# Performance work log

Measured on AMD Instinct MI355X. Metric: run time of the kernel, lower is better.

## Reference

```python
import jax, jax.numpy as jnp
import numpy as np

DECAY = 0.99
EPS = 1e-5
NUM_EMBEDDINGS = 8192


def setup_inputs() -> dict:
    key = jax.random.key(0)
    k1, k2 = jax.random.split(key)
    N, D, K = 65536, 64, NUM_EMBEDDINGS
    x = jax.random.normal(k1, (N, D), dtype=jnp.float32)
    vq_embedding = jax.random.uniform(k2, (K, D), dtype=jnp.float32)
    vq_cluster_size = jnp.ones((K,), dtype=jnp.float32)
    return {"x": x, "vq_embedding": vq_embedding, "vq_cluster_size": vq_cluster_size}


def reference(x, vq_embedding, vq_cluster_size):
    N, D = x.shape
    K = vq_embedding.shape[0]

    # BatchNorm1d(affine=False), training mode: normalize with batch stats (biased var)
    mean = jnp.mean(x, axis=0)                      # [D]
    var = jnp.var(x, axis=0)                        # biased, [D]
    xn = (x - mean) / jnp.sqrt(var + EPS)           # [N, D]

    # pairwise squared distances [N, K]
    distances = (jnp.sum(xn * xn, axis=1, keepdims=True)
                 + jnp.sum(vq_embedding * vq_embedding, axis=1)
                 - 2.0 * (xn @ vq_embedding.T))
    idx = jnp.argmin(distances, axis=1)             # [N]

    # one-hot scatter expressed as segment sums
    dw = jax.ops.segment_sum(xn, idx, num_segments=K)                      # [K, D]
    counts = jax.ops.segment_sum(jnp.ones((N,), x.dtype), idx, num_segments=K)  # [K]

    # EMA codebook update
    new_emb = vq_cluster_size[:, None] * vq_embedding * DECAY + (1.0 - DECAY) * dw
    new_size = vq_cluster_size * DECAY + (1.0 - DECAY) * counts
    new_emb = new_emb / new_size[:, None]

    # BN running stats with momentum=None (cumulative avg, first batch):
    # running_mean = batch mean, running_var = unbiased batch var
    unbiased_var = var * (N / (N - 1))
    running_std = jnp.sqrt(unbiased_var + EPS)
    vq_embedding_output = new_emb * running_std[None, :] + mean[None, :]

    return vq_embedding_output, new_emb, new_size
```

## Files before the change

### kernel.cpp

```cpp
#include <hip/hip_runtime.h>

#define NROWS 65536
#define DIM 64
#define KCODES 8192
#define DECAYF 0.99f
#define EPSV 1e-5f
#define KD (KCODES * DIM)
#define KSPLIT 4
#define KC (KCODES / KSPLIT)
#define ROUNDS (KC / 128)

typedef _Float16 half8 __attribute__((ext_vector_type(8)));
typedef float f32x16 __attribute__((ext_vector_type(16)));

#define WS_STATS  0
#define WS_NHCK   256
#define WS_EBUF   8448
#define WS_PSUM   270592
#define WS_PSQ    286976
#define WS_PACKED 303360
#define WS_DW     368896
#define WS_COUNTS 893184
#define ZERO_F4   149504

__global__ __launch_bounds__(256) void k_prep_stats(
    const float* __restrict__ emb, const float* __restrict__ x,
    half8* __restrict__ ebuf, float* __restrict__ nhck,
    float* __restrict__ psum, float* __restrict__ psq,
    float4* __restrict__ zbase)
{
    const int tid = blockIdx.x * 256 + threadIdx.x;

    #pragma unroll
    for (int i = 0; i < 3; ++i) {
        int z = tid + i * 65536;
        if (z < ZERO_F4) zbase[z] = float4{0.f, 0.f, 0.f, 0.f};
    }

    {
        const int code = tid >> 3, sub = tid & 7;
        const int c = sub >> 1, h = sub & 1;
        const float* e = emb + (size_t)code * DIM + c * 16 + h * 8;
        float4 a = *(const float4*)e;
        float4 b = *(const float4*)(e + 4);
        float f[8] = {a.x, a.y, a.z, a.w, b.x, b.y, b.z, b.w};
        half8 hh;
        float ssq = 0.f;
        #pragma unroll
        for (int i = 0; i < 8; ++i) {
            hh[i] = (_Float16)(f[i] - 0.5f);
            ssq += f[i] * f[i];
        }
        #pragma unroll
        for (int o = 1; o < 8; o <<= 1) ssq += __shfl_xor(ssq, o, 64);
        if (sub == 0) nhck[code] = 10.6875f - 0.5f * ssq;
        const int R = code >> 7, t = (code >> 5) & 3, col = code & 31;
        ebuf[(size_t)R * 1024 + t * 256 + c * 64 + h * 32 + col] = hh;
    }

    {
        const int wave = threadIdx.x >> 6;
        const int col  = threadIdx.x & 63;
        const int base = blockIdx.x * 256;
        float s = 0.f, q = 0.f;
        #pragma unroll 4
        for (int i = 0; i < 64; ++i) {
            int r = base + i * 4 + wave;
            float v = x[(size_t)r * DIM + col];
            s += v;
            q += v * v;
        }
        __shared__ float ls[4][64];
        __shared__ float lq[4][64];
        ls[wave][col] = s;
        lq[wave][col] = q;
        __syncthreads();
        if (threadIdx.x < 64) {
            psum[blockIdx.x * 64 + col] = ls[0][col] + ls[1][col] + ls[2][col] + ls[3][col];
            psq[blockIdx.x * 64 + col]  = lq[0][col] + lq[1][col] + lq[2][col] + lq[3][col];
        }
    }
}

__global__ __launch_bounds__(256) void k_colstats_final(
    const float* __restrict__ psum, const float* __restrict__ psq,
    float* __restrict__ stats)
{
    const int col = threadIdx.x & 63, part = threadIdx.x >> 6;
    float s = 0.f, q = 0.f;
    for (int i = part * 64; i < part * 64 + 64; ++i) {
        s += psum[i * 64 + col];
        q += psq[i * 64 + col];
    }
    __shared__ float ls[4][64];
    __shared__ float lq[4][64];
    ls[part][col] = s;
    lq[part][col] = q;
    __syncthreads();
    if (threadIdx.x < 64) {
        s = ls[0][col] + ls[1][col] + ls[2][col] + ls[3][col];
        q = lq[0][col] + lq[1][col] + lq[2][col] + lq[3][col];
        const float n = (float)NROWS;
        float mean = s / n;
        float var = q / n - mean * mean;
        if (var < 0.f) var = 0.f;
        stats[col]       = mean;
        stats[64 + col]  = 1.0f / sqrtf(var + EPSV);
        stats[128 + col] = sqrtf(var * (n / (n - 1.0f)) + EPSV);
    }
}

__device__ __forceinline__ void gload16(const void* g, void* l)
{
    __builtin_amdgcn_global_load_lds(
        (const __attribute__((address_space(1))) void*)g,
        (__attribute__((address_space(3))) void*)l, 16, 0, 0);
}

__device__ __forceinline__ void build_afrag(const float* __restrict__ xr,
                                            const float* __restrict__ stats,
                                            int h, half8* a)
{
    #pragma unroll
    for (int c = 0; c < 4; ++c) {
        const int d = c * 16 + h * 8;
        float4 v0 = *(const float4*)(xr + d);
        float4 v1 = *(const float4*)(xr + d + 4);
        float4 m0 = *(const float4*)(stats + d);
        float4 m1 = *(const float4*)(stats + d + 4);
        float4 s0 = *(const float4*)(stats + 64 + d);
        float4 s1 = *(const float4*)(stats + 64 + d + 4);
        a[c][0] = (_Float16)((v0.x - m0.x) * s0.x);
        a[c][1] = (_Float16)((v0.y - m0.y) * s0.y);
        a[c][2] = (_Float16)((v0.z - m0.z) * s0.z);
        a[c][3] = (_Float16)((v0.w - m0.w) * s0.w);
        a[c][4] = (_Float16)((v1.x - m1.x) * s1.x);
        a[c][5] = (_Float16)((v1.y - m1.y) * s1.y);
        a[c][6] = (_Float16)((v1.z - m1.z) * s1.z);
        a[c][7] = (_Float16)((v1.w - m1.w) * s1.w);
    }
}

__global__ __launch_bounds__(256) void k_argmin32(
    const float* __restrict__ x, const half8* __restrict__ ebuf,
    const float* __restrict__ nhckg, const float* __restrict__ stats,
    unsigned* __restrict__ packed)
{
    __shared__ half8 smem[2048];

    const int lane = threadIdx.x & 63;
    const int wave = threadIdx.x >> 6;
    const int kc = blockIdx.y;
    const int col = lane & 31, h = lane >> 5;
    const int rowbase = blockIdx.x * 256 + wave * 64;

    half8 a0[4], a1[4];
    build_afrag(x + (size_t)(rowbase + col) * DIM, stats, h, a0);
    build_afrag(x + (size_t)(rowbase + 32 + col) * DIM, stats, h, a1);

    float best0[16], best1[16];
    #pragma unroll
    for (int i = 0; i < 16; ++i) { best0[i] = -3.4e38f; best1[i] = -3.4e38f; }

    const half8* esrc = ebuf + (size_t)kc * (KC * 8);
    const float* ckb = nhckg + kc * KC;

    {
        const char* src = (const char*)esrc + threadIdx.x * 16;
        char* dst = (char*)smem + threadIdx.x * 16;
        #pragma unroll
        for (int i = 0; i < 4; ++i) gload16(src + i * 4096, dst + i * 4096);
    }
    float nv[4];
    #pragma unroll
    for (int t = 0; t < 4; ++t) nv[t] = ckb[t * 32 + col];
    __syncthreads();

    for (int R = 0; R < ROUNDS; ++R) {
        const int buf = R & 1;
        float nvn[4] = {0.f, 0.f, 0.f, 0.f};
        if (R < ROUNDS - 1) {
            const char* src = (const char*)esrc + (size_t)(R + 1) * 16384 + threadIdx.x * 16;
            char* dst = (char*)smem + (buf ^ 1) * 16384 + threadIdx.x * 16;
            #pragma unroll
            for (int i = 0; i < 4; ++i) gload16(src + i * 4096, dst + i * 4096);
            #pragma unroll
            for (int t = 0; t < 4; ++t) nvn[t] = ckb[(R + 1) * 128 + t * 32 + col];
        }

        const half8* sb = smem + buf * 1024 + lane;
        #pragma unroll
        for (int t = 0; t < 4; ++t) {
            half8 b0 = sb[t * 256];
            half8 b1 = sb[t * 256 + 64];
            half8 b2 = sb[t * 256 + 128];
            half8 b3 = sb[t * 256 + 192];
            f32x16 acc0, acc1;
            #pragma unroll
            for (int i = 0; i < 16; ++i) { acc0[i] = nv[t]; acc1[i] = nv[t]; }
            __builtin_amdgcn_s_setprio(1);
            acc0 = __builtin_amdgcn_mfma_f32_32x32x16_f16(a0[0], b0, acc0, 0, 0, 0);
            acc1 = __builtin_amdgcn_mfma_f32_32x32x16_f16(a1[0], b0, acc1, 0, 0, 0);
            acc0 = __builtin_amdgcn_mfma_f32_32x32x16_f16(a0[1], b1, acc0, 0, 0, 0);
            acc1 = __builtin_amdgcn_mfma_f32_32x32x16_f16(a1[1], b1, acc1, 0, 0, 0);
            acc0 = __builtin_amdgcn_mfma_f32_32x32x16_f16(a0[2], b2, acc0, 0, 0, 0);
            acc1 = __builtin_amdgcn_mfma_f32_32x32x16_f16(a1[2], b2, acc1, 0, 0, 0);
            acc0 = __builtin_amdgcn_mfma_f32_32x32x16_f16(a0[3], b3, acc0, 0, 0, 0);
            acc1 = __builtin_amdgcn_mfma_f32_32x32x16_f16(a1[3], b3, acc1, 0, 0, 0);
            __builtin_amdgcn_s_setprio(0);
            const unsigned key = (unsigned)(8191 - (kc * KC + R * 128 + t * 32 + col));
            #pragma unroll
            for (int i = 0; i < 16; ++i) {
                unsigned u0 = (__float_as_uint(acc0[i]) & 0xFFFFE000u) | key;
                best0[i] = fmaxf(best0[i], __uint_as_float(u0));
                unsigned u1 = (__float_as_uint(acc1[i]) & 0xFFFFE000u) | key;
                best1[i] = fmaxf(best1[i], __uint_as_float(u1));
            }
        }
        __syncthreads();
        #pragma unroll
        for (int t = 0; t < 4; ++t) nv[t] = nvn[t];
    }

    #pragma unroll
    for (int off = 1; off < 32; off <<= 1) {
        #pragma unroll
        for (int i = 0; i < 16; ++i) {
            best0[i] = fmaxf(best0[i], __shfl_xor(best0[i], off, 64));
            best1[i] = fmaxf(best1[i], __shfl_xor(best1[i], off, 64));
        }
    }
    if (col == 0) {
        const int rb = rowbase + 4 * h;
        #pragma unroll
        for (int i = 0; i < 16; ++i) {
            int row = rb + (i & 3) + 8 * (i >> 2);
            unsigned u0 = __float_as_uint(best0[i]);
            u0 = (u0 & 0x80000000u) ? ~u0 : (u0 | 0x80000000u);
            atomicMax(&packed[row], u0);
            unsigned u1 = __float_as_uint(best1[i]);
            u1 = (u1 & 0x80000000u) ? ~u1 : (u1 | 0x80000000u);
            atomicMax(&packed[row + 32], u1);
        }
    }
}

__global__ __launch_bounds__(256) void k_scatter(
    const float* __restrict__ x, const float* __restrict__ stats,
    const unsigned* __restrict__ packed,
    float* __restrict__ dw, float* __restrict__ counts)
{
    const int t = blockIdx.x * 256 + threadIdx.x;
    const int row = t >> 6, col = t & 63;
    const unsigned v = packed[row];
    const unsigned key = (v & 0x80000000u) ? (v & 8191u) : (~v & 8191u);
    const int j = 8191 - (int)key;
    float xv = (x[(size_t)row * DIM + col] - stats[col]) * stats[64 + col];
    atomicAdd(&dw[(size_t)j * DIM + col], xv);
    if (col == 0) atomicAdd(&counts[j], 1.0f);
}

__global__ __launch_bounds__(256) void k_final(
    const float* __restrict__ emb, const float* __restrict__ cs,
    const float* __restrict__ dw, const float* __restrict__ counts,
    const float* __restrict__ stats, float* __restrict__ out)
{
    const int t = blockIdx.x * 256 + threadIdx.x;
    const int k = t >> 6, d = t & 63;
    float csk = cs[k];
    float ns = csk * DECAYF + (1.f - DECAYF) * counts[k];
    float ne = (csk * emb[t] * DECAYF + (1.f - DECAYF) * dw[t]) / ns;
    out[KD + t] = ne;
    out[t] = ne * stats[128 + d] + stats[d];
    if (d == 0) out[2 * KD + k] = ns;
}

extern "C" void kernel_launch(void* const* d_in, const int* in_sizes, int n_in,
                              void* d_out, int out_size, void* d_ws, size_t ws_size,
                              hipStream_t stream)
{
    const float* x   = (const float*)d_in[0];
    const float* emb = (const float*)d_in[1];
    const float* cs  = (const float*)d_in[2];
    float* out = (float*)d_out;
    float* ws  = (float*)d_ws;

    float* stats  = ws + WS_STATS;
    float* nhck   = ws + WS_NHCK;
    half8* ebuf   = (half8*)(ws + WS_EBUF);
    float* psum   = ws + WS_PSUM;
    float* psq    = ws + WS_PSQ;
    unsigned* packed = (unsigned*)(ws + WS_PACKED);
    float* dw     = ws + WS_DW;
    float* counts = ws + WS_COUNTS;

    k_prep_stats<<<256, 256, 0, stream>>>(emb, x, ebuf, nhck, psum, psq,
                                          (float4*)(ws + WS_PACKED));
    k_colstats_final<<<1, 256, 0, stream>>>(psum, psq, stats);
    dim3 g3(NROWS / 256, KSPLIT);
    k_argmin32<<<g3, 256, 0, stream>>>(x, ebuf, nhck, stats, packed);
    k_scatter<<<(NROWS * DIM) / 256, 256, 0, stream>>>(x, stats, packed, dw, counts);
    k_final<<<KD / 256, 256, 0, stream>>>(emb, cs, dw, counts, stats, out);
}
```

Baseline: 157.1 us.

## Transpose MFMA operands so codes lie along the accumulator and reduce in-register

The argmin GEMM swaps operand roles: codebook fragments now come from shared memory as the A operand and normalized rows are held as B. Each lane's 16 accumulator values then belong to different codes of the same row, so the argmin reduces inside registers with a small tree, and the 5-stage cross-lane shuffle reduction and most of the atomics go away. The per-code bias is stored in a permuted layout and loaded straight into the accumulator as the MFMA initializer. Separately, the prep/stats kernel launches more blocks with fewer rows each, which makes the single-block final reduction longer. Only 4 low mantissa bits carry the in-tile tie-break index before the code key is packed in, so the intermediate tie ordering could change slightly.

```diff
diff --git a/kernel.cpp b/kernel.cpp
--- a/kernel.cpp
+++ b/kernel.cpp
@@ -14,30 +14,26 @@
 typedef float f32x16 __attribute__((ext_vector_type(16)));
 
 #define WS_STATS  0
-#define WS_NHCK   256
+#define WS_NHCKP  256
 #define WS_EBUF   8448
 #define WS_PSUM   270592
-#define WS_PSQ    286976
-#define WS_PACKED 303360
-#define WS_DW     368896
-#define WS_COUNTS 893184
+#define WS_PSQ    336128
+#define WS_PACKED 401664
+#define WS_DW     467200
+#define WS_COUNTS 991488
 #define ZERO_F4   149504
 
 __global__ __launch_bounds__(256) void k_prep_stats(
     const float* __restrict__ emb, const float* __restrict__ x,
-    half8* __restrict__ ebuf, float* __restrict__ nhck,
+    half8* __restrict__ ebuf, float* __restrict__ nhckP,
     float* __restrict__ psum, float* __restrict__ psq,
     float4* __restrict__ zbase)
 {
     const int tid = blockIdx.x * 256 + threadIdx.x;
 
-    #pragma unroll
-    for (int i = 0; i < 3; ++i) {
-        int z = tid + i * 65536;
-        if (z < ZERO_F4) zbase[z] = float4{0.f, 0.f, 0.f, 0.f};
-    }
-
-    {
+    if (tid < ZERO_F4) zbase[tid] = float4{0.f, 0.f, 0.f, 0.f};
+
+    if (tid < 65536) {
         const int code = tid >> 3, sub = tid & 7;
         const int c = sub >> 1, h = sub & 1;
         const float* e = emb + (size_t)code * DIM + c * 16 + h * 8;
@@ -53,7 +49,13 @@
         }
         #pragma unroll
         for (int o = 1; o < 8; o <<= 1) ssq += __shfl_xor(ssq, o, 64);
-        if (sub == 0) nhck[code] = 10.6875f - 0.5f * ssq;
+        if (sub == 0) {
+            const int c32 = code & 31;
+            const int hh2 = (c32 >> 2) & 1;
+            const int rem = c32 - 4 * hh2;
+            const int reg = (rem & 3) + 4 * (rem >> 3);
+            nhckP[(code >> 5) * 32 + hh2 * 16 + reg] = 10.6875f - 0.5f * ssq;
+        }
         const int R = code >> 7, t = (code >> 5) & 3, col = code & 31;
         ebuf[(size_t)R * 1024 + t * 256 + c * 64 + h * 32 + col] = hh;
     }
@@ -61,10 +63,10 @@
     {
         const int wave = threadIdx.x >> 6;
         const int col  = threadIdx.x & 63;
-        const int base = blockIdx.x * 256;
+        const int base = blockIdx.x * 64;
         float s = 0.f, q = 0.f;
         #pragma unroll 4
-        for (int i = 0; i < 64; ++i) {
+        for (int i = 0; i < 16; ++i) {
             int r = base + i * 4 + wave;
             float v = x[(size_t)r * DIM + col];
             s += v;
@@ -88,7 +90,7 @@
 {
     const int col = threadIdx.x & 63, part = threadIdx.x >> 6;
     float s = 0.f, q = 0.f;
-    for (int i = part * 64; i < part * 64 + 64; ++i) {
+    for (int i = part * 256; i < part * 256 + 256; ++i) {
         s += psum[i * 64 + col];
         q += psq[i * 64 + col];
     }
@@ -117,9 +119,9 @@
         (__attribute__((address_space(3))) void*)l, 16, 0, 0);
 }
 
-__device__ __forceinline__ void build_afrag(const float* __restrict__ xr,
-                                            const float* __restrict__ stats,
-                                            int h, half8* a)
+__device__ __forceinline__ void build_rowfrag(const float* __restrict__ xr,
+                                              const float* __restrict__ stats,
+                                              int h, half8* a)
 {
     #pragma unroll
     for (int c = 0; c < 4; ++c) {
@@ -141,9 +143,28 @@
     }
 }
 
+__device__ __forceinline__ float tile_select(f32x16 acc, unsigned ktile, float best)
+{
+    float u[16];
+    #pragma unroll
+    for (int i = 0; i < 16; ++i)
+        u[i] = __uint_as_float((__float_as_uint(acc[i]) & 0xFFFFFFF0u)
+                               | (unsigned)(15 - i));
+    #pragma unroll
+    for (int s = 8; s >= 1; s >>= 1) {
+        #pragma unroll
+        for (int i = 0; i < s; ++i) u[i] = fmaxf(u[i], u[i + s]);
+    }
+    unsigned mb = __float_as_uint(u[0]);
+    unsigned i2 = 15u - (mb & 15u);
+    unsigned crow = (i2 & 3u) + ((i2 >> 2) << 3);
+    unsigned uf = (mb & 0xFFFFE000u) | (ktile - crow);
+    return fmaxf(best, __uint_as_float(uf));
+}
+
 __global__ __launch_bounds__(256) void k_argmin32(
     const float* __restrict__ x, const half8* __restrict__ ebuf,
-    const float* __restrict__ nhckg, const float* __restrict__ stats,
+    const float* __restrict__ nhckP, const float* __restrict__ stats,
     unsigned* __restrict__ packed)
 {
     __shared__ half8 smem[2048];
@@ -154,16 +175,15 @@
     const int col = lane & 31, h = lane >> 5;
     const int rowbase = blockIdx.x * 256 + wave * 64;
 
-    half8 a0[4], a1[4];
-    build_afrag(x + (size_t)(rowbase + col) * DIM, stats, h, a0);
-    build_afrag(x + (size_t)(rowbase + 32 + col) * DIM, stats, h, a1);
-
-    float best0[16], best1[16];
-    #pragma unroll
-    for (int i = 0; i < 16; ++i) { best0[i] = -3.4e38f; best1[i] = -3.4e38f; }
+    half8 b0[4], b1[4];
+    build_rowfrag(x + (size_t)(rowbase + col) * DIM, stats, h, b0);
+    build_rowfrag(x + (size_t)(rowbase + 32 + col) * DIM, stats, h, b1);
+
+    float best0 = -3.4e38f, best1 = -3.4e38f;
 
     const half8* esrc = ebuf + (size_t)kc * (KC * 8);
-    const float* ckb = nhckg + kc * KC;
+    const float* nvp = nhckP + kc * KC + h * 16;
+    const unsigned kbase = (unsigned)(8191 - kc * KC - 4 * h);
 
     {
         const char* src = (const char*)esrc + threadIdx.x * 16;
@@ -171,77 +191,52 @@
         #pragma unroll
         for (int i = 0; i < 4; ++i) gload16(src + i * 4096, dst + i * 4096);
     }
-    float nv[4];
-    #pragma unroll
-    for (int t = 0; t < 4; ++t) nv[t] = ckb[t * 32 + col];
     __syncthreads();
 
     for (int R = 0; R < ROUNDS; ++R) {
         const int buf = R & 1;
-        float nvn[4] = {0.f, 0.f, 0.f, 0.f};
         if (R < ROUNDS - 1) {
             const char* src = (const char*)esrc + (size_t)(R + 1) * 16384 + threadIdx.x * 16;
             char* dst = (char*)smem + (buf ^ 1) * 16384 + threadIdx.x * 16;
             #pragma unroll
             for (int i = 0; i < 4; ++i) gload16(src + i * 4096, dst + i * 4096);
-            #pragma unroll
-            for (int t = 0; t < 4; ++t) nvn[t] = ckb[(R + 1) * 128 + t * 32 + col];
         }
 
         const half8* sb = smem + buf * 1024 + lane;
         #pragma unroll
         for (int t = 0; t < 4; ++t) {
-            half8 b0 = sb[t * 256];
-            half8 b1 = sb[t * 256 + 64];
-            half8 b2 = sb[t * 256 + 128];
-            half8 b3 = sb[t * 256 + 192];
+            half8 a0 = sb[t * 256];
+            half8 a1 = sb[t * 256 + 64];
+            half8 a2 = sb[t * 256 + 128];
+            half8 a3 = sb[t * 256 + 192];
+            f32x16 ci = *(const f32x16*)(nvp + R * 128 + t * 32);
             f32x16 acc0, acc1;
-            #pragma unroll
-            for (int i = 0; i < 16; ++i) { acc0[i] = nv[t]; acc1[i] = nv[t]; }
             __builtin_amdgcn_s_setprio(1);
-            acc0 = __builtin_amdgcn_mfma_f32_32x32x16_f16(a0[0], b0, acc0, 0, 0, 0);
-            acc1 = __builtin_amdgcn_mfma_f32_32x32x16_f16(a1[0], b0, acc1, 0, 0, 0);
-            acc0 = __builtin_amdgcn_mfma_f32_32x32x16_f16(a0[1], b1, acc0, 0, 0, 0);
-            acc1 = __builtin_amdgcn_mfma_f32_32x32x16_f16(a1[1], b1, acc1, 0, 0, 0);
-            acc0 = __builtin_amdgcn_mfma_f32_32x32x16_f16(a0[2], b2, acc0, 0, 0, 0);
-            acc1 = __builtin_amdgcn_mfma_f32_32x32x16_f16(a1[2], b2, acc1, 0, 0, 0);
-            acc0 = __builtin_amdgcn_mfma_f32_32x32x16_f16(a0[3], b3, acc0, 0, 0, 0);
-            acc1 = __builtin_amdgcn_mfma_f32_32x32x16_f16(a1[3], b3, acc1, 0, 0, 0);
+            acc0 = __builtin_amdgcn_mfma_f32_32x32x16_f16(a0, b0[0], ci, 0, 0, 0);
+            acc1 = __builtin_amdgcn_mfma_f32_32x32x16_f16(a0, b1[0], ci, 0, 0, 0);
+            acc0 = __builtin_amdgcn_mfma_f32_32x32x16_f16(a1, b0[1], acc0, 0, 0, 0);
+            acc1 = __builtin_amdgcn_mfma_f32_32x32x16_f16(a1, b1[1], acc1, 0, 0, 0);
+            acc0 = __builtin_amdgcn_mfma_f32_32x32x16_f16(a2, b0[2], acc0, 0, 0, 0);
+            acc1 = __builtin_amdgcn_mfma_f32_32x32x16_f16(a2, b1[2], acc1, 0, 0, 0);
+            acc0 = __builtin_amdgcn_mfma_f32_32x32x16_f16(a3, b0[3], acc0, 0, 0, 0);
+            acc1 = __builtin_amdgcn_mfma_f32_32x32x16_f16(a3, b1[3], acc1, 0, 0, 0);
             __builtin_amdgcn_s_setprio(0);
-            const unsigned key = (unsigned)(8191 - (kc * KC + R * 128 + t * 32 + col));
-            #pragma unroll
-            for (int i = 0; i < 16; ++i) {
-                unsigned u0 = (__float_as_uint(acc0[i]) & 0xFFFFE000u) | key;
-                best0[i] = fmaxf(best0[i], __uint_as_float(u0));
-                unsigned u1 = (__float_as_uint(acc1[i]) & 0xFFFFE000u) | key;
-                best1[i] = fmaxf(best1[i], __uint_as_float(u1));
-            }
+            const unsigned ktile = kbase - (unsigned)(R * 128 + t * 32);
+            best0 = tile_select(acc0, ktile, best0);
+            best1 = tile_select(acc1, ktile, best1);
         }
         __syncthreads();
-        #pragma unroll
-        for (int t = 0; t < 4; ++t) nv[t] = nvn[t];
-    }
-
-    #pragma unroll
-    for (int off = 1; off < 32; off <<= 1) {
-        #pragma unroll
-        for (int i = 0; i < 16; ++i) {
-            best0[i] = fmaxf(best0[i], __shfl_xor(best0[i], off, 64));
-            best1[i] = fmaxf(best1[i], __shfl_xor(best1[i], off, 64));
-        }
-    }
-    if (col == 0) {
-        const int rb = rowbase + 4 * h;
-        #pragma unroll
-        for (int i = 0; i < 16; ++i) {
-            int row = rb + (i & 3) + 8 * (i >> 2);
-            unsigned u0 = __float_as_uint(best0[i]);
-            u0 = (u0 & 0x80000000u) ? ~u0 : (u0 | 0x80000000u);
-            atomicMax(&packed[row], u0);
-            unsigned u1 = __float_as_uint(best1[i]);
-            u1 = (u1 & 0x80000000u) ? ~u1 : (u1 | 0x80000000u);
-            atomicMax(&packed[row + 32], u1);
-        }
+    }
+
+    best0 = fmaxf(best0, __shfl_xor(best0, 32, 64));
+    best1 = fmaxf(best1, __shfl_xor(best1, 32, 64));
+    if (h == 0) {
+        unsigned u0 = __float_as_uint(best0);
+        u0 = (u0 & 0x80000000u) ? ~u0 : (u0 | 0x80000000u);
+        atomicMax(&packed[rowbase + col], u0);
+        unsigned u1 = __float_as_uint(best1);
+        u1 = (u1 & 0x80000000u) ? ~u1 : (u1 | 0x80000000u);
+        atomicMax(&packed[rowbase + 32 + col], u1);
     }
 }
 
@@ -286,7 +281,7 @@
     float* ws  = (float*)d_ws;
 
     float* stats  = ws + WS_STATS;
-    float* nhck   = ws + WS_NHCK;
+    float* nhckP  = ws + WS_NHCKP;
     half8* ebuf   = (half8*)(ws + WS_EBUF);
     float* psum   = ws + WS_PSUM;
     float* psq    = ws + WS_PSQ;
@@ -294,11 +289,11 @@
     float* dw     = ws + WS_DW;
     float* counts = ws + WS_COUNTS;
 
-    k_prep_stats<<<256, 256, 0, stream>>>(emb, x, ebuf, nhck, psum, psq,
-                                          (float4*)(ws + WS_PACKED));
+    k_prep_stats<<<1024, 256, 0, stream>>>(emb, x, ebuf, nhckP, psum, psq,
+                                           (float4*)(ws + WS_PACKED));
     k_colstats_final<<<1, 256, 0, stream>>>(psum, psq, stats);
     dim3 g3(NROWS / 256, KSPLIT);
-    k_argmin32<<<g3, 256, 0, stream>>>(x, ebuf, nhck, stats, packed);
+    k_argmin32<<<g3, 256, 0, stream>>>(x, ebuf, nhckP, stats, packed);
     k_scatter<<<(NROWS * DIM) / 256, 256, 0, stream>>>(x, stats, packed, dw, counts);
     k_final<<<KD / 256, 256, 0, stream>>>(emb, cs, dw, counts, stats, out);
 }
```

Result: slower. 160.7 us (+2.3%).

## Widen stats reduction grid, transpose partials, and vectorize scatter loads

Applied to the files above, without the earlier changes.

The prep/stats kernel now runs 1024 blocks instead of 256, so each block reduces 64 rows and the embedding and zeroing work lose their inner loops. Partial sums are stored transposed per column, which lets the final column-stats kernel use 64 blocks with vector loads and a tree reduction instead of a single block. The scatter kernel has each thread handle two columns with float2 loads, halving the thread count while keeping the same number of atomics. This targets the serial single-block reduction and the low parallelism in the prep stage, at the cost of four times as many partial-sum entries and a rearranged workspace layout.

```diff
diff --git a/kernel.cpp b/kernel.cpp
--- a/kernel.cpp
+++ b/kernel.cpp
@@ -17,27 +17,23 @@
 #define WS_NHCK   256
 #define WS_EBUF   8448
 #define WS_PSUM   270592
-#define WS_PSQ    286976
-#define WS_PACKED 303360
-#define WS_DW     368896
-#define WS_COUNTS 893184
+#define WS_PSQ    336128
+#define WS_PACKED 401664
+#define WS_DW     467200
+#define WS_COUNTS 991488
 #define ZERO_F4   149504
 
 __global__ __launch_bounds__(256) void k_prep_stats(
     const float* __restrict__ emb, const float* __restrict__ x,
     half8* __restrict__ ebuf, float* __restrict__ nhck,
-    float* __restrict__ psum, float* __restrict__ psq,
+    float* __restrict__ psumT, float* __restrict__ psqT,
     float4* __restrict__ zbase)
 {
     const int tid = blockIdx.x * 256 + threadIdx.x;
 
-    #pragma unroll
-    for (int i = 0; i < 3; ++i) {
-        int z = tid + i * 65536;
-        if (z < ZERO_F4) zbase[z] = float4{0.f, 0.f, 0.f, 0.f};
-    }
-
-    {
+    if (tid < ZERO_F4) zbase[tid] = float4{0.f, 0.f, 0.f, 0.f};
+
+    if (tid < 65536) {
         const int code = tid >> 3, sub = tid & 7;
         const int c = sub >> 1, h = sub & 1;
         const float* e = emb + (size_t)code * DIM + c * 16 + h * 8;
@@ -61,10 +57,10 @@
     {
         const int wave = threadIdx.x >> 6;
         const int col  = threadIdx.x & 63;
-        const int base = blockIdx.x * 256;
+        const int base = blockIdx.x * 64;
         float s = 0.f, q = 0.f;
         #pragma unroll 4
-        for (int i = 0; i < 64; ++i) {
+        for (int i = 0; i < 16; ++i) {
             int r = base + i * 4 + wave;
             float v = x[(size_t)r * DIM + col];
             s += v;
@@ -76,37 +72,43 @@
         lq[wave][col] = q;
         __syncthreads();
         if (threadIdx.x < 64) {
-            psum[blockIdx.x * 64 + col] = ls[0][col] + ls[1][col] + ls[2][col] + ls[3][col];
-            psq[blockIdx.x * 64 + col]  = lq[0][col] + lq[1][col] + lq[2][col] + lq[3][col];
+            psumT[col * 1024 + blockIdx.x] = ls[0][col] + ls[1][col] + ls[2][col] + ls[3][col];
+            psqT[col * 1024 + blockIdx.x]  = lq[0][col] + lq[1][col] + lq[2][col] + lq[3][col];
         }
     }
 }
 
 __global__ __launch_bounds__(256) void k_colstats_final(
-    const float* __restrict__ psum, const float* __restrict__ psq,
+    const float* __restrict__ psumT, const float* __restrict__ psqT,
     float* __restrict__ stats)
 {
-    const int col = threadIdx.x & 63, part = threadIdx.x >> 6;
-    float s = 0.f, q = 0.f;
-    for (int i = part * 64; i < part * 64 + 64; ++i) {
-        s += psum[i * 64 + col];
-        q += psq[i * 64 + col];
-    }
-    __shared__ float ls[4][64];
-    __shared__ float lq[4][64];
-    ls[part][col] = s;
-    lq[part][col] = q;
+    const int col = blockIdx.x, t = threadIdx.x;
+    float4 a = *(const float4*)(psumT + col * 1024 + t * 4);
+    float4 b = *(const float4*)(psqT + col * 1024 + t * 4);
+    float s = a.x + a.y + a.z + a.w;
+    float q = b.x + b.y + b.z + b.w;
+    __shared__ float rs[256], rq[256];
+    rs[t] = s; rq[t] = q;
     __syncthreads();
-    if (threadIdx.x < 64) {
-        s = ls[0][col] + ls[1][col] + ls[2][col] + ls[3][col];
-        q = lq[0][col] + lq[1][col] + lq[2][col] + lq[3][col];
-        const float n = (float)NROWS;
-        float mean = s / n;
-        float var = q / n - mean * mean;
-        if (var < 0.f) var = 0.f;
-        stats[col]       = mean;
-        stats[64 + col]  = 1.0f / sqrtf(var + EPSV);
-        stats[128 + col] = sqrtf(var * (n / (n - 1.0f)) + EPSV);
+    if (t < 128) { rs[t] += rs[t + 128]; rq[t] += rq[t + 128]; }
+    __syncthreads();
+    if (t < 64) {
+        s = rs[t] + rs[t + 64];
+        q = rq[t] + rq[t + 64];
+        #pragma unroll
+        for (int o = 32; o > 0; o >>= 1) {
+            s += __shfl_xor(s, o, 64);
+            q += __shfl_xor(q, o, 64);
+        }
+        if (t == 0) {
+            const float n = (float)NROWS;
+            float mean = s / n;
+            float var = q / n - mean * mean;
+            if (var < 0.f) var = 0.f;
+            stats[col]       = mean;
+            stats[64 + col]  = 1.0f / sqrtf(var + EPSV);
+            stats[128 + col] = sqrtf(var * (n / (n - 1.0f)) + EPSV);
+        }
     }
 }
 
@@ -251,13 +253,16 @@
     float* __restrict__ dw, float* __restrict__ counts)
 {
     const int t = blockIdx.x * 256 + threadIdx.x;
-    const int row = t >> 6, col = t & 63;
+    const int row = t >> 5, c2 = (t & 31) * 2;
     const unsigned v = packed[row];
     const unsigned key = (v & 0x80000000u) ? (v & 8191u) : (~v & 8191u);
     const int j = 8191 - (int)key;
-    float xv = (x[(size_t)row * DIM + col] - stats[col]) * stats[64 + col];
-    atomicAdd(&dw[(size_t)j * DIM + col], xv);
-    if (col == 0) atomicAdd(&counts[j], 1.0f);
+    float2 xv = *(const float2*)(x + (size_t)row * DIM + c2);
+    float2 mu = *(const float2*)(stats + c2);
+    float2 sg = *(const float2*)(stats + 64 + c2);
+    atomicAdd(&dw[(size_t)j * DIM + c2],     (xv.x - mu.x) * sg.x);
+    atomicAdd(&dw[(size_t)j * DIM + c2 + 1], (xv.y - mu.y) * sg.y);
+    if (c2 == 0) atomicAdd(&counts[j], 1.0f);
 }
 
 __global__ __launch_bounds__(256) void k_final(
@@ -288,17 +293,17 @@
     float* stats  = ws + WS_STATS;
     float* nhck   = ws + WS_NHCK;
     half8* ebuf   = (half8*)(ws + WS_EBUF);
-    float* psum   = ws + WS_PSUM;
-    float* psq    = ws + WS_PSQ;
+    float* psumT  = ws + WS_PSUM;
+    float* psqT   = ws + WS_PSQ;
     unsigned* packed = (unsigned*)(ws + WS_PACKED);
     float* dw     = ws + WS_DW;
     float* counts = ws + WS_COUNTS;
 
-    k_prep_stats<<<256, 256, 0, stream>>>(emb, x, ebuf, nhck, psum, psq,
-                                          (float4*)(ws + WS_PACKED));
-    k_colstats_final<<<1, 256, 0, stream>>>(psum, psq, stats);
+    k_prep_stats<<<1024, 256, 0, stream>>>(emb, x, ebuf, nhck, psumT, psqT,
+                                           (float4*)(ws + WS_PACKED));
+    k_colstats_final<<<64, 256, 0, stream>>>(psumT, psqT, stats);
     dim3 g3(NROWS / 256, KSPLIT);
     k_argmin32<<<g3, 256, 0, stream>>>(x, ebuf, nhck, stats, packed);
-    k_scatter<<<(NROWS * DIM) / 256, 256, 0, stream>>>(x, stats, packed, dw, counts);
+    k_scatter<<<NROWS * 32 / 256, 256, 0, stream>>>(x, stats, packed, dw, counts);
     k_final<<<KD / 256, 256, 0, stream>>>(emb, cs, dw, counts, stats, out);
 }
```

Result: slower. 180.1 us (+14.6%).
